# Kernel tuning notes

Hardware: AMD Instinct MI355X
Metric: run time of the kernel (lower is better)

## Reference

```python
import jax, jax.numpy as jnp
import numpy as np

# Model hyperparameters (match init_kwargs)
N_HEADS = 16
N_KV_HEADS = 4
HEAD_DIM = 128
ROPE_THETA = 10000.0
WINDOW = 1024  # sliding window (left), right window = 0
SOFTCAP = 50.0
B, T, C = 2, 2048, 2048
G = N_HEADS // N_KV_HEADS


def _sine_table(features, length, max_timescale):
    # min_timescale = 1.0 in the original
    fraction = jnp.arange(0, features, 2, dtype=jnp.float32) / features
    inv_timescale = 1.0 / (max_timescale ** fraction)
    sinusoid = jnp.einsum('i,j->ij', jnp.arange(length), inv_timescale,
                          precision=jax.lax.Precision.HIGHEST)
    sinusoid = jnp.concatenate([sinusoid, sinusoid], axis=-1)  # [T, H]
    return jnp.sin(sinusoid), jnp.cos(sinusoid)


def _rotate_half(x):
    x1, x2 = jnp.split(x, 2, axis=-1)
    return jnp.concatenate([-x2, x1], axis=-1)


def setup_inputs() -> dict:
    key = jax.random.key(0)
    kx, kq, kk, kv, ko = jax.random.split(key, 5)
    x = jax.random.normal(kx, (B, T, C), dtype=jnp.float32)
    init = lambda k, shape: 0.02 * jax.random.normal(k, shape, dtype=jnp.float32)
    q_kernel = init(kq, (C, N_HEADS * HEAD_DIM))
    k_kernel = init(kk, (C, N_KV_HEADS * HEAD_DIM))
    v_kernel = init(kv, (C, N_KV_HEADS * HEAD_DIM))
    out_kernel = init(ko, (N_HEADS * HEAD_DIM, C))
    return {"x": x, "q_kernel": q_kernel, "k_kernel": k_kernel,
            "v_kernel": v_kernel, "out_kernel": out_kernel}


def _attention(x, q_kernel, k_kernel, v_kernel, out_kernel):
    Bs, Ts, Cs = x.shape
    K, H, Gn = N_KV_HEADS, HEAD_DIM, G
    q = jnp.dot(x, q_kernel).reshape(Bs, Ts, K, Gn, H)
    k = jnp.dot(x, k_kernel).reshape(Bs, Ts, K, H)
    v = jnp.dot(x, v_kernel).reshape(Bs, Ts, K, H)

    # RoPE: cos/sin broadcast along the T axis (axis 1), over heads.
    sin, cos = _sine_table(H, Ts, ROPE_THETA)
    qcos = cos[None, :, None, None, :]
    qsin = sin[None, :, None, None, :]
    kcos = cos[None, :, None, :]
    ksin = sin[None, :, None, :]
    q = (q * qcos + _rotate_half(q) * qsin).astype(q.dtype)
    k = (k * kcos + _rotate_half(k) * ksin).astype(k.dtype)

    # Causal + sliding-window mask: key <= query <= key + WINDOW
    pos = jnp.arange(Ts)
    mask = (pos[:, None] >= pos[None, :]) & (pos[:, None] <= pos[None, :] + WINDOW)
    mask = mask[None, None, :, :]  # [1,1,T,S]
    neg = jnp.asarray(-0.7 * jnp.finfo(jnp.float32).max, dtype=jnp.float32)

    scale = jnp.asarray(H ** (-0.5), dtype=q.dtype)
    encoded = []
    for i in range(Gn):  # fixed, small group loop (matches GQA structure)
        qi = q[:, :, :, i] * scale                              # [B,T,K,H]
        logits = jnp.einsum('BTKH,BSKH->BKTS', qi, k)
        logits = jnp.tanh(logits / SOFTCAP) * SOFTCAP           # softcap
        logits = jnp.where(mask, logits, neg)
        probs = jax.nn.softmax(logits.astype(jnp.float32), axis=-1).astype(logits.dtype)
        encoded.append(jnp.einsum('BKTS,BSKH->BTKH', probs, v))
    encoded = jnp.stack(encoded, axis=3)                        # [B,T,K,G,H]
    encoded = encoded.reshape(Bs, Ts, N_HEADS * H)
    return jnp.dot(encoded, out_kernel)


def reference(x, q_kernel, k_kernel, v_kernel, out_kernel):
    return _attention(x, q_kernel, k_kernel, v_kernel, out_kernel)
```

## Files before the change

kernel.cpp:

```cpp
#include <hip/hip_runtime.h>
#include <hip/hip_bf16.h>
#include <math.h>

#define BB 2
#define TT 2048
#define CC 2048
#define NH 16
#define NKV 4
#define HD 128
#define BT (BB*TT)
#define WINDOW 1024
#define SQKV 3072

typedef unsigned short u16;
typedef unsigned int u32;
typedef __attribute__((ext_vector_type(8))) short short8;
typedef __attribute__((ext_vector_type(8))) unsigned short ushort8;
typedef __attribute__((ext_vector_type(4))) unsigned short ushort4v;
typedef __attribute__((ext_vector_type(2))) unsigned int uint2v;
typedef __attribute__((ext_vector_type(4))) float floatx4;
typedef __attribute__((ext_vector_type(16))) float floatx16;

typedef const __attribute__((address_space(1))) u32* gas_ptr;
typedef __attribute__((address_space(3))) u32* las_ptr;

static __device__ __forceinline__ u16 f2bf(float f) {
    unsigned u = __builtin_bit_cast(unsigned, f);
    return (u16)((u + 0x7fffu + ((u >> 16) & 1u)) >> 16);
}
static __device__ __forceinline__ float bf2f(u16 v) {
    unsigned u = ((unsigned)v) << 16;
    return __builtin_bit_cast(float, u);
}

static __device__ __forceinline__ u32 cvt_pk_bf16(float lo, float hi) {
    u32 r;
    asm("v_cvt_pk_bf16_f32 %0, %1, %2" : "=v"(r) : "v"(lo), "v"(hi));
    return r;
}

static __device__ __forceinline__ float softcap_exp(float s) {
    float t = s * 0.02f;
    t = fmaxf(-1.0f, fminf(1.0f, t));
    float t2 = t * t;
    float e = t * fmaf(t2, fmaf(t2, 9.617967f, -24.044917f), 72.134752f);
    return __builtin_amdgcn_exp2f(e);
}

__global__ void cast_bf16_kernel(const float* __restrict__ in, u16* __restrict__ out, int n4) {
    int i = blockIdx.x * blockDim.x + threadIdx.x;
    if (i >= n4) return;
    floatx4 v = *(const floatx4*)(in + (size_t)i * 4);
    ushort4v o;
    o[0] = f2bf(v[0]); o[1] = f2bf(v[1]); o[2] = f2bf(v[2]); o[3] = f2bf(v[3]);
    *(ushort4v*)(out + (size_t)i * 4) = o;
}

__global__ void transpose_cast_f32_kernel(const float* __restrict__ in, u16* __restrict__ out,
                                          int R, int Cc) {
    __shared__ u16 tile[32][33];
    int c0 = blockIdx.x * 32, r0 = blockIdx.y * 32;
    int tx = threadIdx.x, ty = threadIdx.y;
    #pragma unroll
    for (int i = 0; i < 4; i++) {
        int r = r0 + ty + i * 8;
        tile[ty + i * 8][tx] = f2bf(in[(size_t)r * Cc + c0 + tx]);
    }
    __syncthreads();
    #pragma unroll
    for (int i = 0; i < 4; i++) {
        int c = c0 + ty + i * 8;
        out[(size_t)c * R + r0 + tx] = tile[tx][ty + i * 8];
    }
}

__global__ void transpose_bf16_kernel(const u16* __restrict__ in, u16* __restrict__ out,
                                      int R, int Cc, int inStride, int colOff,
                                      size_t inBatchStride, size_t outBatchStride) {
    __shared__ u16 tile[32][33];
    int b = blockIdx.z;
    const u16* inb = in + (size_t)b * inBatchStride;
    u16* outb = out + (size_t)b * outBatchStride;
    int c0 = blockIdx.y * 32, r0 = blockIdx.x * 32;
    int tx = threadIdx.x, ty = threadIdx.y;
    #pragma unroll
    for (int i = 0; i < 4; i++) {
        int r = r0 + ty + i * 8;
        tile[ty + i * 8][tx] = inb[(size_t)r * inStride + colOff + c0 + tx];
    }
    __syncthreads();
    #pragma unroll
    for (int i = 0; i < 4; i++) {
        int c = c0 + ty + i * 8;
        outb[(size_t)c * R + r0 + tx] = tile[tx][ty + i * 8];
    }
}

__global__ void rope_kernel(u16* __restrict__ buf, int H, int rowStride, float scale) {
    int idx = blockIdx.x;
    int bt = idx / H, h = idx - bt * H;
    int t = bt % TT;
    int d = threadIdx.x;
    u16* p = buf + (size_t)bt * rowStride + h * HD;
    float x  = bf2f(p[d]);
    float xp = bf2f(p[d ^ 64]);
    int j = d & 63;
    float inv = exp2f(-0.20762050593046f * (float)j);
    float ang = (float)t * inv;
    float s, c;
    sincosf(ang, &s, &c);
    float rot = (d < 64) ? -xp : xp;
    float o = (x * c + rot * s) * scale;
    __syncthreads();
    p[d] = f2bf(o);
}

template <bool OUT_F32>
__global__ __launch_bounds__(256) void gemm128_kernel(const u16* __restrict__ A,
                                                      const u16* __restrict__ Bt,
                                                      void* __restrict__ Cout,
                                                      int M, int N, int K) {
    __shared__ alignas(16) u16 As[128 * 32];
    __shared__ alignas(16) u16 Bs[128 * 32];
    int tid = threadIdx.x;
    int w = tid >> 6, lane = tid & 63, quad = lane >> 4, ln = lane & 15;
    int m0 = blockIdx.y * 128;
    int n0 = blockIdx.x * 128;
    int wm = (w >> 1) * 64;
    int wn = (w & 1) * 64;

    int o0 = (w * 2) * 1024 + lane * 16;
    int row0 = o0 >> 6, kc0 = (o0 & 63) >> 4;
    int o1 = o0 + 1024;
    int row1 = o1 >> 6, kc1 = (o1 & 63) >> 4;
    const u16* gA0 = A  + (size_t)(m0 + row0) * K + kc0 * 8;
    const u16* gA1 = A  + (size_t)(m0 + row1) * K + kc1 * 8;
    const u16* gB0 = Bt + (size_t)(n0 + row0) * K + kc0 * 8;
    const u16* gB1 = Bt + (size_t)(n0 + row1) * K + kc1 * 8;
    u16* lA0 = As + (w * 2) * 512;
    u16* lA1 = As + (w * 2 + 1) * 512;
    u16* lB0 = Bs + (w * 2) * 512;
    u16* lB1 = Bs + (w * 2 + 1) * 512;

    floatx4 acc[4][4] = {};

    for (int k0 = 0; k0 < K; k0 += 32) {
        __syncthreads();
        __builtin_amdgcn_global_load_lds((gas_ptr)(gA0 + k0), (las_ptr)lA0, 16, 0, 0);
        __builtin_amdgcn_global_load_lds((gas_ptr)(gA1 + k0), (las_ptr)lA1, 16, 0, 0);
        __builtin_amdgcn_global_load_lds((gas_ptr)(gB0 + k0), (las_ptr)lB0, 16, 0, 0);
        __builtin_amdgcn_global_load_lds((gas_ptr)(gB1 + k0), (las_ptr)lB1, 16, 0, 0);
        __syncthreads();

        short8 af[4], bf[4];
        #pragma unroll
        for (int mt = 0; mt < 4; mt++)
            af[mt] = *(const short8*)(As + (wm + mt * 16 + ln) * 32 + quad * 8);
        #pragma unroll
        for (int nt = 0; nt < 4; nt++)
            bf[nt] = *(const short8*)(Bs + (wn + nt * 16 + ln) * 32 + quad * 8);
        #pragma unroll
        for (int mt = 0; mt < 4; mt++)
            #pragma unroll
            for (int nt = 0; nt < 4; nt++)
                acc[mt][nt] = __builtin_amdgcn_mfma_f32_16x16x32_bf16(af[mt], bf[nt], acc[mt][nt], 0, 0, 0);
    }

    #pragma unroll
    for (int mt = 0; mt < 4; mt++)
      #pragma unroll
      for (int nt = 0; nt < 4; nt++)
        #pragma unroll
        for (int r = 0; r < 4; r++) {
            size_t row = m0 + wm + mt * 16 + quad * 4 + r;
            size_t col = n0 + wn + nt * 16 + ln;
            float v = acc[mt][nt][r];
            if (OUT_F32) ((float*)Cout)[row * N + col] = v;
            else         ((u16*)Cout)[row * N + col] = f2bf(v);
        }
}

__global__ __launch_bounds__(256, 2) void attn_kernel(const u16* __restrict__ QKV,
                                                      const u16* __restrict__ Vt,
                                                      u16* __restrict__ Enc) {
    __shared__ alignas(16) u16 pool[2 * 8192];

    int tid = threadIdx.x;
    int w = tid >> 6, lane = tid & 63, hi = lane >> 5, ln = lane & 31;
    int hi8 = hi * 8;

    int qb = (15 - (int)blockIdx.x) * 128;
    int bh = blockIdx.y;
    int b = bh >> 4, h = bh & 15, kh = h >> 2;
    int qw = qb + w * 32;

    short8 qf[8];
    {
        const u16* qptr = QKV + (size_t)(b * TT + qw + ln) * SQKV + h * HD + hi8;
        #pragma unroll
        for (int ks = 0; ks < 8; ks++) qf[ks] = *(const short8*)(qptr + ks * 16);
    }

    int sig = (ln & 3) + (((ln >> 3) & 1) << 2) + (((ln >> 2) & 1) << 3) + ((ln >> 4) << 4);
    bool isK = (w < 2);
    const u16* dsrc[4];
    int ldst[4];
    #pragma unroll
    for (int i = 0; i < 4; i++) {
        if (isK) {
            int ks = w * 4 + i;
            dsrc[i] = QKV + (size_t)(b * TT + sig) * SQKV + 2048 + kh * HD + ks * 16 + hi8;
            ldst[i] = ks * 512;
        } else {
            int g = (w - 2) * 4 + i;
            dsrc[i] = Vt + (size_t)((b * NKV + kh) * HD + (g >> 1) * 32 + ln) * TT + (g & 1) * 16 + hi8;
            ldst[i] = 4096 + g * 512;
        }
    }
    size_t addmul = isK ? (size_t)SQKV : (size_t)1;

    floatx16 O0 = {}, O1 = {}, O2 = {}, O3 = {};
    float lacc = 0.0f;

    int S_LO = qb - WINDOW; if (S_LO < 0) S_LO = 0;
    int nt = (qb + 128 - S_LO) >> 5;

    auto issue = [&](int t) {
        int s0 = S_LO + t * 32;
        u16* base = pool + (t & 1) * 8192;
        size_t add = (size_t)s0 * addmul;
        #pragma unroll
        for (int i = 0; i < 4; i++)
            __builtin_amdgcn_global_load_lds((gas_ptr)(dsrc[i] + add), (las_ptr)(base + ldst[i]), 16, 0, 0);
    };

    issue(0);
    for (int t = 0; t < nt; ++t) {
        __builtin_amdgcn_sched_barrier(0);
        __builtin_amdgcn_s_barrier();
        __builtin_amdgcn_sched_barrier(0);
        if (t + 1 < nt) {
            issue(t + 1);
            __builtin_amdgcn_sched_barrier(0);
            __builtin_amdgcn_s_waitcnt(0x0F74);
        } else {
            __builtin_amdgcn_s_waitcnt(0x0F70);
        }
        __builtin_amdgcn_sched_barrier(0);
        __builtin_amdgcn_s_barrier();
        __builtin_amdgcn_sched_barrier(0);

        int s0 = S_LO + t * 32;
        if (s0 > qw + 31 || s0 + 31 < qw - WINDOW) continue;

        const u16* Kb = pool + (t & 1) * 8192;
        const u16* Vb = Kb + 4096;

        floatx16 S = {};
        #pragma unroll
        for (int ks = 0; ks < 8; ks++) {
            short8 kf = *(const short8*)(Kb + ks * 512 + lane * 8);
            S = __builtin_amdgcn_mfma_f32_32x32x16_bf16(kf, qf[ks], S, 0, 0, 0);
        }

        bool full = (s0 + 31 <= qw) && (s0 >= qw + 31 - WINDOW);
        if (full) {
            #pragma unroll
            for (int r = 0; r < 16; r++) S[r] = softcap_exp(S[r]);
        } else {
            int tq = qw + ln;
            #pragma unroll
            for (int r = 0; r < 16; r++) {
                int s = s0 + (r & 3) + (((r >> 2) & 1) << 2) + hi8 + ((r >> 3) << 4);
                bool good = (s <= tq) && (s >= tq - WINDOW);
                S[r] = good ? softcap_exp(S[r]) : 0.0f;
            }
        }

        lacc += ((((S[0] + S[1]) + (S[2] + S[3])) + ((S[4] + S[5]) + (S[6] + S[7])))
               + (((S[8] + S[9]) + (S[10] + S[11])) + ((S[12] + S[13]) + (S[14] + S[15]))));

        u32 w0a = cvt_pk_bf16(S[0],  S[1]),  w0b = cvt_pk_bf16(S[2],  S[3]);
        u32 w0c = cvt_pk_bf16(S[4],  S[5]),  w0d = cvt_pk_bf16(S[6],  S[7]);
        u32 w1a = cvt_pk_bf16(S[8],  S[9]),  w1b = cvt_pk_bf16(S[10], S[11]);
        u32 w1c = cvt_pk_bf16(S[12], S[13]), w1d = cvt_pk_bf16(S[14], S[15]);
        typedef __attribute__((ext_vector_type(4))) unsigned int u32x4t;
        u32x4t pw0 = { w0a, w0b, w0c, w0d };
        u32x4t pw1 = { w1a, w1b, w1c, w1d };
        short8 pf0 = __builtin_bit_cast(short8, pw0);
        short8 pf1 = __builtin_bit_cast(short8, pw1);

        #pragma unroll
        for (int dt = 0; dt < 4; dt++) {
            short8 vf0 = *(const short8*)(Vb + (dt * 2 + 0) * 512 + lane * 8);
            short8 vf1 = *(const short8*)(Vb + (dt * 2 + 1) * 512 + lane * 8);
            floatx16* Od = (dt == 0) ? &O0 : (dt == 1) ? &O1 : (dt == 2) ? &O2 : &O3;
            *Od = __builtin_amdgcn_mfma_f32_32x32x16_bf16(vf0, pf0, *Od, 0, 0, 0);
            *Od = __builtin_amdgcn_mfma_f32_32x32x16_bf16(vf1, pf1, *Od, 0, 0, 0);
        }
    }

    __syncthreads();

    lacc += __shfl_xor(lacc, 32);
    float inv = __builtin_amdgcn_rcpf(lacc);
    u16* ep = pool + w * 1024;
    const floatx16* Os[4] = { &O0, &O1, &O2, &O3 };
    #pragma unroll
    for (int dt = 0; dt < 4; dt++) {
        #pragma unroll
        for (int g = 0; g < 4; g++) {
            float a0 = (*Os[dt])[g * 4 + 0] * inv, a1 = (*Os[dt])[g * 4 + 1] * inv;
            float a2 = (*Os[dt])[g * 4 + 2] * inv, a3 = (*Os[dt])[g * 4 + 3] * inv;
            uint2v pk;
            pk[0] = cvt_pk_bf16(a0, a1);
            pk[1] = cvt_pk_bf16(a2, a3);
            *(uint2v*)(ep + ln * 32 + g * 8 + hi * 4) = pk;
        }
        ushort8 r0 = *(const ushort8*)(ep + ln * 32 + hi * 16);
        ushort8 r1 = *(const ushort8*)(ep + ln * 32 + hi * 16 + 8);
        u16* dst = Enc + (size_t)(b * TT + qw + ln) * (NH * HD) + h * HD + dt * 32 + hi * 16;
        *(ushort8*)dst = r0;
        *(ushort8*)(dst + 8) = r1;
    }
}

extern "C" void kernel_launch(void* const* d_in, const int* in_sizes, int n_in,
                              void* d_out, int out_size, void* d_ws, size_t ws_size,
                              hipStream_t stream) {
    const float* x  = (const float*)d_in[0];
    const float* wq = (const float*)d_in[1];
    const float* wk = (const float*)d_in[2];
    const float* wv = (const float*)d_in[3];
    const float* wo = (const float*)d_in[4];
    float* out = (float*)d_out;

    char* ws = (char*)d_ws;
    size_t off = 0;
    auto alloc = [&](size_t bytes) -> void* {
        void* p = ws + off;
        off += (bytes + 255) & ~(size_t)255;
        return p;
    };
    u16* xb    = (u16*)alloc((size_t)BT * CC * 2);
    u16* wqkvT = (u16*)alloc((size_t)SQKV * CC * 2);
    u16* woT   = (u16*)alloc((size_t)CC * CC * 2);
    u16* QKVb  = (u16*)alloc((size_t)BT * SQKV * 2);
    u16* VtT   = (u16*)alloc((size_t)BT * NKV * HD * 2);
    u16* Enc   = (u16*)alloc((size_t)BT * NH * HD * 2);

    cast_bf16_kernel<<<(BT * CC / 4 + 255) / 256, 256, 0, stream>>>(x, xb, BT * CC / 4);
    dim3 tb(32, 8);
    transpose_cast_f32_kernel<<<dim3(CC / 32, CC / 32), tb, 0, stream>>>(wq, wqkvT, CC, CC);
    transpose_cast_f32_kernel<<<dim3(NKV * HD / 32, CC / 32), tb, 0, stream>>>(wk, wqkvT + (size_t)2048 * CC, CC, NKV * HD);
    transpose_cast_f32_kernel<<<dim3(NKV * HD / 32, CC / 32), tb, 0, stream>>>(wv, wqkvT + (size_t)2560 * CC, CC, NKV * HD);
    transpose_cast_f32_kernel<<<dim3(CC / 32, CC / 32), tb, 0, stream>>>(wo, woT, CC, CC);

    gemm128_kernel<false><<<dim3(SQKV / 128, BT / 128), 256, 0, stream>>>(xb, wqkvT, QKVb, BT, SQKV, CC);

    rope_kernel<<<BT * NH, HD, 0, stream>>>(QKVb, NH, SQKV, 0.08838834764831845f);
    rope_kernel<<<BT * NKV, HD, 0, stream>>>(QKVb + 2048, NKV, SQKV, 1.0f);

    transpose_bf16_kernel<<<dim3(TT / 32, NKV * HD / 32, BB), tb, 0, stream>>>(
        QKVb, VtT, TT, NKV * HD, SQKV, 2560,
        (size_t)TT * SQKV, (size_t)NKV * HD * TT);

    attn_kernel<<<dim3(16, 32), 256, 0, stream>>>(QKVb, VtT, Enc);

    gemm128_kernel<true><<<dim3(CC / 128, BT / 128), 256, 0, stream>>>(Enc, woT, out, BT, CC, CC);
}
```

Measured before the change: 329.6 us.

## Fuse V transpose into QKV GEMM epilogue and vectorize RoPE with trig table

The QKV GEMM epilogue now writes the V columns straight into a transposed Vt buffer, which removes the separate bf16 transpose kernel. RoPE is rewritten so each block handles one token row across all heads, using vectorized 4-element loads and a precomputed cos/sin table instead of a per-element sincos. The aim is to drop one full pass over V and reduce the launch count and transcendental cost of RoPE. In exchange, an extra table-build kernel runs every call, and the V portion of QKVb is no longer written.

```diff
diff --git a/kernel.cpp b/kernel.cpp
--- a/kernel.cpp
+++ b/kernel.cpp
@@ -74,51 +74,43 @@
     }
 }
 
-__global__ void transpose_bf16_kernel(const u16* __restrict__ in, u16* __restrict__ out,
-                                      int R, int Cc, int inStride, int colOff,
-                                      size_t inBatchStride, size_t outBatchStride) {
-    __shared__ u16 tile[32][33];
-    int b = blockIdx.z;
-    const u16* inb = in + (size_t)b * inBatchStride;
-    u16* outb = out + (size_t)b * outBatchStride;
-    int c0 = blockIdx.y * 32, r0 = blockIdx.x * 32;
-    int tx = threadIdx.x, ty = threadIdx.y;
+__global__ void trig_table_kernel(float* __restrict__ tab) {
+    int t = blockIdx.x, j = threadIdx.x;
+    float inv = exp2f(-0.20762050593046f * (float)j);
+    float s, c;
+    sincosf((float)t * inv, &s, &c);
+    float* p = tab + (t * 64 + j) * 2;
+    p[0] = c; p[1] = s;
+}
+
+__global__ void rope_fast_kernel(u16* __restrict__ buf, const float* __restrict__ tab,
+                                 int rowStride, float scale) {
+    int bt = blockIdx.x;
+    int t = bt & (TT - 1);
+    int tid = threadIdx.x;
+    int h = tid >> 4;
+    int j0 = (tid & 15) * 4;
+    u16* p = buf + (size_t)bt * rowStride + h * HD + j0;
+    ushort4v lo = *(const ushort4v*)(p);
+    ushort4v hi = *(const ushort4v*)(p + 64);
+    const float* tb = tab + (t * 64 + j0) * 2;
+    ushort4v olo, ohi;
     #pragma unroll
     for (int i = 0; i < 4; i++) {
-        int r = r0 + ty + i * 8;
-        tile[ty + i * 8][tx] = inb[(size_t)r * inStride + colOff + c0 + tx];
-    }
-    __syncthreads();
-    #pragma unroll
-    for (int i = 0; i < 4; i++) {
-        int c = c0 + ty + i * 8;
-        outb[(size_t)c * R + r0 + tx] = tile[tx][ty + i * 8];
-    }
-}
-
-__global__ void rope_kernel(u16* __restrict__ buf, int H, int rowStride, float scale) {
-    int idx = blockIdx.x;
-    int bt = idx / H, h = idx - bt * H;
-    int t = bt % TT;
-    int d = threadIdx.x;
-    u16* p = buf + (size_t)bt * rowStride + h * HD;
-    float x  = bf2f(p[d]);
-    float xp = bf2f(p[d ^ 64]);
-    int j = d & 63;
-    float inv = exp2f(-0.20762050593046f * (float)j);
-    float ang = (float)t * inv;
-    float s, c;
-    sincosf(ang, &s, &c);
-    float rot = (d < 64) ? -xp : xp;
-    float o = (x * c + rot * s) * scale;
-    __syncthreads();
-    p[d] = f2bf(o);
-}
-
-template <bool OUT_F32>
+        float c = tb[2 * i], s = tb[2 * i + 1];
+        float x1 = bf2f(lo[i]), x2 = bf2f(hi[i]);
+        olo[i] = f2bf((x1 * c - x2 * s) * scale);
+        ohi[i] = f2bf((x2 * c + x1 * s) * scale);
+    }
+    *(ushort4v*)(p) = olo;
+    *(ushort4v*)(p + 64) = ohi;
+}
+
+template <int OMODE>
 __global__ __launch_bounds__(256) void gemm128_kernel(const u16* __restrict__ A,
                                                       const u16* __restrict__ Bt,
                                                       void* __restrict__ Cout,
+                                                      u16* __restrict__ Vt,
                                                       int M, int N, int K) {
     __shared__ alignas(16) u16 As[128 * 32];
     __shared__ alignas(16) u16 Bs[128 * 32];
@@ -166,18 +158,34 @@
                 acc[mt][nt] = __builtin_amdgcn_mfma_f32_16x16x32_bf16(af[mt], bf[nt], acc[mt][nt], 0, 0, 0);
     }
 
-    #pragma unroll
-    for (int mt = 0; mt < 4; mt++)
-      #pragma unroll
-      for (int nt = 0; nt < 4; nt++)
-        #pragma unroll
-        for (int r = 0; r < 4; r++) {
-            size_t row = m0 + wm + mt * 16 + quad * 4 + r;
-            size_t col = n0 + wn + nt * 16 + ln;
-            float v = acc[mt][nt][r];
-            if (OUT_F32) ((float*)Cout)[row * N + col] = v;
-            else         ((u16*)Cout)[row * N + col] = f2bf(v);
-        }
+    if (OMODE == 2 && n0 >= 2560) {
+        int b = m0 >> 11;
+        int tb = (m0 & (TT - 1)) + wm;
+        #pragma unroll
+        for (int mt = 0; mt < 4; mt++)
+          #pragma unroll
+          for (int nt = 0; nt < 4; nt++) {
+              int c = n0 + wn + nt * 16 + ln - 2560;
+              int t0 = tb + mt * 16 + quad * 4;
+              ushort4v o;
+              #pragma unroll
+              for (int r = 0; r < 4; r++) o[r] = f2bf(acc[mt][nt][r]);
+              *(ushort4v*)(Vt + (size_t)b * (NKV * HD) * TT + (size_t)c * TT + t0) = o;
+          }
+    } else {
+        #pragma unroll
+        for (int mt = 0; mt < 4; mt++)
+          #pragma unroll
+          for (int nt = 0; nt < 4; nt++)
+            #pragma unroll
+            for (int r = 0; r < 4; r++) {
+                size_t row = m0 + wm + mt * 16 + quad * 4 + r;
+                size_t col = n0 + wn + nt * 16 + ln;
+                float v = acc[mt][nt][r];
+                if (OMODE == 1) ((float*)Cout)[row * N + col] = v;
+                else            ((u16*)Cout)[row * N + col] = f2bf(v);
+            }
+    }
 }
 
 __global__ __launch_bounds__(256, 2) void attn_kernel(const u16* __restrict__ QKV,
@@ -348,6 +356,9 @@
     u16* QKVb  = (u16*)alloc((size_t)BT * SQKV * 2);
     u16* VtT   = (u16*)alloc((size_t)BT * NKV * HD * 2);
     u16* Enc   = (u16*)alloc((size_t)BT * NH * HD * 2);
+    float* trig = (float*)alloc((size_t)TT * 64 * 2 * 4);
+
+    trig_table_kernel<<<TT, 64, 0, stream>>>(trig);
 
     cast_bf16_kernel<<<(BT * CC / 4 + 255) / 256, 256, 0, stream>>>(x, xb, BT * CC / 4);
     dim3 tb(32, 8);
@@ -356,16 +367,12 @@
     transpose_cast_f32_kernel<<<dim3(NKV * HD / 32, CC / 32), tb, 0, stream>>>(wv, wqkvT + (size_t)2560 * CC, CC, NKV * HD);
     transpose_cast_f32_kernel<<<dim3(CC / 32, CC / 32), tb, 0, stream>>>(wo, woT, CC, CC);
 
-    gemm128_kernel<false><<<dim3(SQKV / 128, BT / 128), 256, 0, stream>>>(xb, wqkvT, QKVb, BT, SQKV, CC);
-
-    rope_kernel<<<BT * NH, HD, 0, stream>>>(QKVb, NH, SQKV, 0.08838834764831845f);
-    rope_kernel<<<BT * NKV, HD, 0, stream>>>(QKVb + 2048, NKV, SQKV, 1.0f);
-
-    transpose_bf16_kernel<<<dim3(TT / 32, NKV * HD / 32, BB), tb, 0, stream>>>(
-        QKVb, VtT, TT, NKV * HD, SQKV, 2560,
-        (size_t)TT * SQKV, (size_t)NKV * HD * TT);
+    gemm128_kernel<2><<<dim3(SQKV / 128, BT / 128), 256, 0, stream>>>(xb, wqkvT, QKVb, VtT, BT, SQKV, CC);
+
+    rope_fast_kernel<<<BT, NH * 16, 0, stream>>>(QKVb, trig, SQKV, 0.08838834764831845f);
+    rope_fast_kernel<<<BT, NKV * 16, 0, stream>>>(QKVb + 2048, trig, SQKV, 1.0f);
 
     attn_kernel<<<dim3(16, 32), 256, 0, stream>>>(QKVb, VtT, Enc);
 
-    gemm128_kernel<true><<<dim3(CC / 128, BT / 128), 256, 0, stream>>>(Enc, woT, out, BT, CC, CC);
-}
+    gemm128_kernel<1><<<dim3(CC / 128, BT / 128), 256, 0, stream>>>(Enc, woT, out, nullptr, BT, CC, CC);
+}
```

Result: faster. 315.4 us (-4.3%).
